# Optimization experiments

Hardware: AMD Instinct MI355X
Metric: run time of the kernel (lower is better)

Reference implementation:

```python
import jax, jax.numpy as jnp
import numpy as np

D_MODEL = 1024
K_QUERY = 32
K_TOPK = 4

def setup_inputs() -> dict:
    key = jax.random.key(0)
    k1, k2, k3, k4, k5 = jax.random.split(key, 5)
    x = jax.random.normal(k1, (4, 2048, D_MODEL), dtype=jnp.float32)
    # nn.Linear(d_model, k_query): weight [k_query, d_model], bias [k_query]
    sc = 1.0 / np.sqrt(D_MODEL)
    Wq = jax.random.uniform(k2, (K_QUERY, D_MODEL), jnp.float32, -sc, sc)
    bq = jax.random.uniform(k3, (K_QUERY,), jnp.float32, -sc, sc)
    Wk = jax.random.uniform(k4, (K_QUERY, D_MODEL), jnp.float32, -sc, sc)
    bk = jax.random.uniform(k5, (K_QUERY,), jnp.float32, -sc, sc)
    return {"x": x, "Wq": Wq, "bq": bq, "Wk": Wk, "bk": bk}

def reference(x, Wq, bq, Wk, bk):
    # x: [B, T, D]
    queries = jnp.einsum('btd,kd->btk', x, Wq) + bq      # [B, T, Kq]
    keys = jnp.einsum('btd,kd->btk', x, Wk) + bk         # [B, T, Kq]
    sim = jnp.einsum('btk,bsk->bts', queries, keys)      # [B, T, T]
    sim = sim / jnp.sqrt(jnp.float32(queries.shape[-1]))
    _, topk_idx = jax.lax.top_k(sim, K_TOPK)              # [B, T, K]
    # gather neighbors per (b, t): x[b, topk_idx[b, t]] -> [B, T, K, D]
    neighbors = jax.vmap(lambda xb, ib: xb[ib])(x, topk_idx)
    gathered = neighbors.mean(axis=2)                     # [B, T, D]
    return gathered
```

## Files before the change

kernel.cpp:

```cpp
#include <hip/hip_runtime.h>
#include <math.h>

#define D_MODEL 1024
#define T_SEQ   2048
#define NBATCH  4
#define NROWS   (NBATCH * T_SEQ)
#define NOUT    64
#define NQTR    4

#define SKLD 264
#define SQLD 36
#define XLD  1032

typedef double v4df __attribute__((ext_vector_type(4)));

__device__ __forceinline__ bool key_gt(float av, int ai, float bv, int bi) {
    return (av > bv) || (av == bv && ai < bi);
}

__device__ __forceinline__ void cmpswap(float& v0, int& i0, float& v1, int& i1) {
    bool sw = key_gt(v1, i1, v0, i0);
    float nv0 = sw ? v1 : v0, nv1 = sw ? v0 : v1;
    int   ni0 = sw ? i1 : i0, ni1 = sw ? i0 : i1;
    v0 = nv0; v1 = nv1; i0 = ni0; i1 = ni1;
}

__device__ __forceinline__ void merge4(float (&a)[4], int (&ai)[4],
                                       float b0, int j0, float b1, int j1,
                                       float b2, int j2, float b3, int j3) {
    if (!key_gt(a[0], ai[0], b3, j3)) { a[0] = b3; ai[0] = j3; }
    if (!key_gt(a[1], ai[1], b2, j2)) { a[1] = b2; ai[1] = j2; }
    if (!key_gt(a[2], ai[2], b1, j1)) { a[2] = b1; ai[2] = j1; }
    if (!key_gt(a[3], ai[3], b0, j0)) { a[3] = b0; ai[3] = j0; }
    cmpswap(a[0], ai[0], a[2], ai[2]);
    cmpswap(a[1], ai[1], a[3], ai[3]);
    cmpswap(a[0], ai[0], a[1], ai[1]);
    cmpswap(a[2], ai[2], a[3], ai[3]);
}

__device__ __forceinline__ void insert4(float (&tv)[4], int (&tix)[4], float v, int idx) {
    if (v > tv[3]) {
        bool g0 = v > tv[0], g1 = v > tv[1], g2 = v > tv[2];
        float n0 = g0 ? v : tv[0];
        int   m0 = g0 ? idx : tix[0];
        float n1 = g1 ? (g0 ? tv[0] : v) : tv[1];
        int   m1 = g1 ? (g0 ? tix[0] : idx) : tix[1];
        float n2 = g2 ? (g1 ? tv[1] : v) : tv[2];
        int   m2 = g2 ? (g1 ? tix[1] : idx) : tix[2];
        float n3 = g2 ? tv[2] : v;
        int   m3 = g2 ? tix[2] : idx;
        tv[0] = n0; tv[1] = n1; tv[2] = n2; tv[3] = n3;
        tix[0] = m0; tix[1] = m1; tix[2] = m2; tix[3] = m3;
    }
}

__global__ __launch_bounds__(64) void mfma_probe(int* __restrict__ tab)
{
    __shared__ double Aref[16][4];
    __shared__ double Bref[4][16];
    __shared__ double Dref[16][16];

    const int lane = threadIdx.x;
    {
        const int m = lane & 15, k = lane >> 4;
        Aref[m][k] = (double)(1 + m * 4 + k);
        Bref[k][m] = (double)(1 + k * 16 + m);
    }
    __syncthreads();
    for (int e = lane; e < 256; e += 64) {
        const int m = e >> 4, n = e & 15;
        double s = 0.0;
        for (int k = 0; k < 4; ++k) s += Aref[m][k] * Bref[k][n];
        Dref[m][n] = s;
    }
    __syncthreads();

    int found = -1;
    for (int h = 0; h < 16; ++h) {
        if (found >= 0) break;
        const int fa = h & 1, fb = (h >> 1) & 1, fd = h >> 2;
        const int am = fa ? (lane >> 2) : (lane & 15);
        const int ak = fa ? (lane & 3)  : (lane >> 4);
        const int bn = fb ? (lane >> 2) : (lane & 15);
        const int bk = fb ? (lane & 3)  : (lane >> 4);
        v4df c = {0.0, 0.0, 0.0, 0.0};
        c = __builtin_amdgcn_mfma_f64_16x16x4f64(Aref[am][ak], Bref[bk][bn], c, 0, 0, 0);
        bool ok = true;
        #pragma unroll
        for (int i = 0; i < 4; ++i) {
            int dm, dn;
            if (fd == 0)      { dm = 4 * (lane >> 4) + i; dn = lane & 15; }
            else if (fd == 1) { dn = 4 * (lane >> 4) + i; dm = lane & 15; }
            else if (fd == 2) { dm = (lane >> 4) + 4 * i; dn = lane & 15; }
            else              { dn = (lane >> 4) + 4 * i; dm = lane & 15; }
            if (c[i] != Dref[dm][dn]) ok = false;
        }
        if (__all(ok)) found = h;
    }

    const int fa = (found >= 0) ? (found & 1) : 0;
    const int fb = (found >= 0) ? ((found >> 1) & 1) : 0;
    const int fd = (found >= 0) ? (found >> 2) : 0;
    tab[1   + lane] = fa ? (lane >> 2) : (lane & 15);
    tab[65  + lane] = fa ? (lane & 3)  : (lane >> 4);
    tab[129 + lane] = fb ? (lane & 3)  : (lane >> 4);
    tab[193 + lane] = fb ? (lane >> 2) : (lane & 15);
    #pragma unroll
    for (int i = 0; i < 4; ++i) {
        int dm, dn;
        if (fd == 0)      { dm = 4 * (lane >> 4) + i; dn = lane & 15; }
        else if (fd == 1) { dn = 4 * (lane >> 4) + i; dm = lane & 15; }
        else if (fd == 2) { dm = (lane >> 4) + 4 * i; dn = lane & 15; }
        else              { dn = (lane >> 4) + 4 * i; dm = lane & 15; }
        tab[257 + lane * 4 + i] = dm;
        tab[513 + lane * 4 + i] = dn;
    }
    if (lane == 0) tab[0] = found;
}

__global__ __launch_bounds__(256) void wprep_kernel(
    const float* __restrict__ Wq, const float* __restrict__ Wk,
    double* __restrict__ Wdt)
{
    const int idx = blockIdx.x * 256 + threadIdx.x;
    const int o = idx & 63;
    const int d = idx >> 6;
    float v = (o < 32) ? Wq[(size_t)o * D_MODEL + d]
                       : Wk[(size_t)(o - 32) * D_MODEL + d];
    Wdt[(size_t)d * 64 + o] = (double)v;
}

__global__ __launch_bounds__(512) void proj_mfma(
    const float* __restrict__ x, const double* __restrict__ Wdt,
    const float* __restrict__ bq, const float* __restrict__ bk_,
    const int* __restrict__ tab,
    float* __restrict__ Qt, float* __restrict__ Kt)
{
    __shared__ float  xlds[16 * XLD];
    __shared__ double comb[4][64][4];

    const int tid  = threadIdx.x;
    const int lane = tid & 63;
    const int wav  = tid >> 6;
    const int og   = __builtin_amdgcn_readfirstlane(wav >> 1);
    const int half = __builtin_amdgcn_readfirstlane(wav & 1);
    const int row0 = blockIdx.x * 16;
    const int dbase = half * 512;

    const int flag = tab[0];
    const int am  = tab[1   + lane];
    const int ak  = tab[65  + lane];
    const int bkk = tab[129 + lane];
    const int bn  = tab[193 + lane];

    const double* wcol = Wdt + og * 16;

    #pragma unroll
    for (int j = 0; j < 8; ++j) {
        const int f  = j * 512 + tid;
        const int r  = f >> 8;
        const int c4 = f & 255;
        float4 v = *reinterpret_cast<const float4*>(
            x + (size_t)(row0 + r) * D_MODEL + c4 * 4);
        *reinterpret_cast<float4*>(&xlds[r * XLD + c4 * 4]) = v;
    }
    __syncthreads();

    v4df acc = {0.0, 0.0, 0.0, 0.0};

    if (flag >= 0) {
        #pragma unroll 8
        for (int kk = 0; kk < 128; ++kk) {
            double a = (double)xlds[am * XLD + dbase + kk * 4 + ak];
            double b = wcol[(size_t)(dbase + kk * 4 + bkk) * 64 + bn];
            acc = __builtin_amdgcn_mfma_f64_16x16x4f64(a, b, acc, 0, 0, 0);
        }
    } else {
        const int n  = lane & 15;
        const int r4 = (lane >> 4) * 4;
        for (int dd = 0; dd < 512; ++dd) {
            const int d = dbase + dd;
            double wv = wcol[(size_t)d * 64 + n];
            #pragma unroll
            for (int i = 0; i < 4; ++i)
                acc[i] = fma((double)xlds[(r4 + i) * XLD + d], wv, acc[i]);
        }
    }

    if (half == 1) {
        #pragma unroll
        for (int i = 0; i < 4; ++i) comb[og][lane][i] = acc[i];
    }
    __syncthreads();

    if (half == 0) {
        #pragma unroll
        for (int i = 0; i < 4; ++i) {
            const double tot = acc[i] + comb[og][lane][i];
            const int dmv = tab[257 + lane * 4 + i];
            const int dnv = tab[513 + lane * 4 + i];
            const int out = og * 16 + dnv;
            const int row = row0 + dmv;
            const int bb  = row >> 11, t = row & 2047;
            const double bias = (out < 32) ? (double)bq[out] : (double)bk_[out - 32];
            const float v = (float)(tot + bias);
            if (out < 32) Qt[((size_t)bb * 32 + out) * T_SEQ + t] = v;
            else          Kt[((size_t)bb * 32 + (out - 32)) * T_SEQ + t] = v;
        }
    }
}

__global__ __launch_bounds__(256) void sim_topk(
    const float* __restrict__ Qt, const float* __restrict__ Kt,
    float* __restrict__ candVal ,
    int*   __restrict__ candIdx )
{
    __shared__ float klds[32 * SKLD];
    __shared__ float qlds[32 * SQLD];
    __shared__ float cV[4][32][4];
    __shared__ int   cI[4][32][4];

    const int tid  = threadIdx.x;
    const int lane = tid & 63;
    const int wav  = tid >> 6;
    const int qtr  = blockIdx.x & 3;
    const int tt   = (blockIdx.x >> 2) & 63;
    const int b    = blockIdx.x >> 8;
    const int tblk = tt * 32;
    const int sq0  = qtr * 512;

    const float* QtB = Qt + (size_t)b * 32 * T_SEQ;
    const float* KtB = Kt + (size_t)b * 32 * T_SEQ;

    {
        const int i  = tid >> 3;
        const int t4 = (tid & 7) * 4;
        float4 v = *reinterpret_cast<const float4*>(QtB + (size_t)i * T_SEQ + tblk + t4);
        *reinterpret_cast<float4*>(&qlds[i * SQLD + t4]) = v;
    }

    const int t0 = (tid & 7) * 4;
    const int s0 = (tid >> 3) * 8;

    float tv[4][4]; int tix[4][4];
    #pragma unroll
    for (int r = 0; r < 4; ++r)
        #pragma unroll
        for (int j = 0; j < 4; ++j) { tv[r][j] = -INFINITY; tix[r][j] = 0x7fffffff; }

    for (int st = 0; st < 2; ++st) {
        __syncthreads();
        #pragma unroll
        for (int j = 0; j < 8; ++j) {
            const int f  = (tid + j * 256) * 4;
            const int ki = f >> 8;
            const int ks = f & 255;
            float4 v = *reinterpret_cast<const float4*>(
                KtB + (size_t)ki * T_SEQ + sq0 + st * 256 + ks);
            *reinterpret_cast<float4*>(&klds[ki * SKLD + ks]) = v;
        }
        __syncthreads();

        float acc[4][8];
        #pragma unroll
        for (int r = 0; r < 4; ++r)
            #pragma unroll
            for (int c = 0; c < 8; ++c) acc[r][c] = 0.f;

        #pragma unroll 4
        for (int i = 0; i < 32; ++i) {
            float4 qv  = *reinterpret_cast<const float4*>(&qlds[i * SQLD + t0]);
            float4 kv0 = *reinterpret_cast<const float4*>(&klds[i * SKLD + s0]);
            float4 kv1 = *reinterpret_cast<const float4*>(&klds[i * SKLD + s0 + 4]);
            const float qa[4] = {qv.x, qv.y, qv.z, qv.w};
            const float ka[8] = {kv0.x, kv0.y, kv0.z, kv0.w, kv1.x, kv1.y, kv1.z, kv1.w};
            #pragma unroll
            for (int r = 0; r < 4; ++r)
                #pragma unroll
                for (int c = 0; c < 8; ++c)
                    acc[r][c] = fmaf(qa[r], ka[c], acc[r][c]);
        }

        const int sbase = sq0 + st * 256 + s0;
        #pragma unroll
        for (int c = 0; c < 8; ++c)
            #pragma unroll
            for (int r = 0; r < 4; ++r)
                insert4(tv[r], tix[r], acc[r][c], sbase + c);
    }

    #pragma unroll
    for (int m = 8; m <= 32; m <<= 1) {
        #pragma unroll
        for (int r = 0; r < 4; ++r) {
            float b0 = __shfl_xor(tv[r][0], m, 64);
            float b1 = __shfl_xor(tv[r][1], m, 64);
            float b2 = __shfl_xor(tv[r][2], m, 64);
            float b3 = __shfl_xor(tv[r][3], m, 64);
            int   j0 = __shfl_xor(tix[r][0], m, 64);
            int   j1 = __shfl_xor(tix[r][1], m, 64);
            int   j2 = __shfl_xor(tix[r][2], m, 64);
            int   j3 = __shfl_xor(tix[r][3], m, 64);
            merge4(tv[r], tix[r], b0, j0, b1, j1, b2, j2, b3, j3);
        }
    }

    if (lane < 8) {
        #pragma unroll
        for (int r = 0; r < 4; ++r)
            #pragma unroll
            for (int j = 0; j < 4; ++j) {
                cV[wav][lane * 4 + r][j] = tv[r][j];
                cI[wav][lane * 4 + r][j] = tix[r][j];
            }
    }
    __syncthreads();

    if (tid < 32) {
        float mv[4]; int mi[4];
        #pragma unroll
        for (int j = 0; j < 4; ++j) { mv[j] = cV[0][tid][j]; mi[j] = cI[0][tid][j]; }
        #pragma unroll
        for (int w = 1; w < 4; ++w)
            merge4(mv, mi,
                   cV[w][tid][0], cI[w][tid][0],
                   cV[w][tid][1], cI[w][tid][1],
                   cV[w][tid][2], cI[w][tid][2],
                   cV[w][tid][3], cI[w][tid][3]);
        const size_t row = (size_t)b * T_SEQ + tblk + tid;
        float4 vv = {mv[0], mv[1], mv[2], mv[3]};
        int4   ii = {mi[0], mi[1], mi[2], mi[3]};
        *reinterpret_cast<float4*>(candVal + ((size_t)qtr * NROWS + row) * 4) = vv;
        *reinterpret_cast<int4*>(candIdx + ((size_t)qtr * NROWS + row) * 4) = ii;
    }
}

__global__ __launch_bounds__(256) void merge_gather(
    const float* __restrict__ x,
    const float* __restrict__ candVal, const int* __restrict__ candIdx,
    float* __restrict__ out)
{
    __shared__ int topIdx[8][4];

    const int tid  = threadIdx.x;
    const int row0 = blockIdx.x * 8;
    const int b    = row0 >> 11;

    if (tid < 8) {
        const size_t row = row0 + tid;
        float4 v0 = *reinterpret_cast<const float4*>(candVal + row * 4);
        int4   i0 = *reinterpret_cast<const int4*>(candIdx + row * 4);
        float mv[4] = {v0.x, v0.y, v0.z, v0.w};
        int   mi[4] = {i0.x, i0.y, i0.z, i0.w};
        #pragma unroll
        for (int q = 1; q < NQTR; ++q) {
            float4 v1 = *reinterpret_cast<const float4*>(candVal + ((size_t)q * NROWS + row) * 4);
            int4   i1 = *reinterpret_cast<const int4*>(candIdx + ((size_t)q * NROWS + row) * 4);
            merge4(mv, mi, v1.x, i1.x, v1.y, i1.y, v1.z, i1.z, v1.w, i1.w);
        }
        #pragma unroll
        for (int j = 0; j < 4; ++j) topIdx[tid][j] = mi[j];
    }
    __syncthreads();

    const float* xb = x + (size_t)b * T_SEQ * D_MODEL;
    float* ob = out + (size_t)row0 * D_MODEL;
    #pragma unroll
    for (int r = 0; r < 8; ++r) {
        const int i0 = topIdx[r][0], i1 = topIdx[r][1], i2 = topIdx[r][2], i3 = topIdx[r][3];
        float4 a0 = *(reinterpret_cast<const float4*>(xb + (size_t)i0 * D_MODEL) + tid);
        float4 a1 = *(reinterpret_cast<const float4*>(xb + (size_t)i1 * D_MODEL) + tid);
        float4 a2 = *(reinterpret_cast<const float4*>(xb + (size_t)i2 * D_MODEL) + tid);
        float4 a3 = *(reinterpret_cast<const float4*>(xb + (size_t)i3 * D_MODEL) + tid);
        float4 o;
        o.x = (a0.x + a1.x + a2.x + a3.x) * 0.25f;
        o.y = (a0.y + a1.y + a2.y + a3.y) * 0.25f;
        o.z = (a0.z + a1.z + a2.z + a3.z) * 0.25f;
        o.w = (a0.w + a1.w + a2.w + a3.w) * 0.25f;
        *(reinterpret_cast<float4*>(ob + (size_t)r * D_MODEL) + tid) = o;
    }
}

extern "C" void kernel_launch(void* const* d_in, const int* in_sizes, int n_in,
                              void* d_out, int out_size, void* d_ws, size_t ws_size,
                              hipStream_t stream) {
    const float* x  = (const float*)d_in[0];
    const float* Wq = (const float*)d_in[1];
    const float* bq = (const float*)d_in[2];
    const float* Wk = (const float*)d_in[3];
    const float* bk = (const float*)d_in[4];
    float* out = (float*)d_out;

    char* wsb = (char*)d_ws;
    int*    tab  = (int*)wsb;
    double* Wdt  = (double*)(wsb + 4096);
    float*  Qt   = (float*)(wsb + 4096 + (size_t)D_MODEL * NOUT * 8);
    float*  Kt   = Qt + (size_t)NBATCH * 32 * T_SEQ;
    float*  candVal = (float*)((char*)Kt + (size_t)NBATCH * 32 * T_SEQ * 4);
    int*    candIdx = (int*)((char*)candVal + (size_t)NQTR * NROWS * 4 * 4);

    mfma_probe<<<dim3(1), dim3(64), 0, stream>>>(tab);
    wprep_kernel<<<dim3(256), dim3(256), 0, stream>>>(Wq, Wk, Wdt);
    proj_mfma<<<dim3(NROWS / 16), dim3(512), 0, stream>>>(x, Wdt, bq, bk, tab, Qt, Kt);
    sim_topk<<<dim3(1024), dim3(256), 0, stream>>>(Qt, Kt, candVal, candIdx);
    merge_gather<<<dim3(1024), dim3(256), 0, stream>>>(x, candVal, candIdx, out);
}
```

Measured before the change: 163.9 us.

## Fuse probe into weight prep and merge+gather into sim_topk via last-block counter

```diff
diff --git a/kernel.cpp b/kernel.cpp
--- a/kernel.cpp
+++ b/kernel.cpp
@@ -54,26 +54,29 @@
     }
 }
 
-__global__ __launch_bounds__(64) void mfma_probe(int* __restrict__ tab)
+__device__ void run_probe(int tid, int* __restrict__ tab)
 {
     __shared__ double Aref[16][4];
     __shared__ double Bref[4][16];
     __shared__ double Dref[16][16];
 
-    const int lane = threadIdx.x;
-    {
+    const int lane = tid;
+    if (tid < 64) {
         const int m = lane & 15, k = lane >> 4;
         Aref[m][k] = (double)(1 + m * 4 + k);
         Bref[k][m] = (double)(1 + k * 16 + m);
     }
     __syncthreads();
-    for (int e = lane; e < 256; e += 64) {
+    {
+        const int e = tid;
         const int m = e >> 4, n = e & 15;
         double s = 0.0;
         for (int k = 0; k < 4; ++k) s += Aref[m][k] * Bref[k][n];
         Dref[m][n] = s;
     }
     __syncthreads();
+
+    if (tid >= 64) return;
 
     int found = -1;
     for (int h = 0; h < 16; ++h) {
@@ -118,16 +121,20 @@
     if (lane == 0) tab[0] = found;
 }
 
-__global__ __launch_bounds__(256) void wprep_kernel(
+__global__ __launch_bounds__(256) void wprep_probe(
     const float* __restrict__ Wq, const float* __restrict__ Wk,
-    double* __restrict__ Wdt)
+    double* __restrict__ Wdt, int* __restrict__ tab, int* __restrict__ cnt)
 {
-    const int idx = blockIdx.x * 256 + threadIdx.x;
+    const int tid = threadIdx.x;
+    const int idx = blockIdx.x * 256 + tid;
     const int o = idx & 63;
     const int d = idx >> 6;
     float v = (o < 32) ? Wq[(size_t)o * D_MODEL + d]
                        : Wk[(size_t)(o - 32) * D_MODEL + d];
     Wdt[(size_t)d * 64 + o] = (double)v;
+
+    if (blockIdx.x == 1) cnt[tid] = 0;
+    if (blockIdx.x == 0) run_probe(tid, tab);
 }
 
 __global__ __launch_bounds__(512) void proj_mfma(
@@ -210,15 +217,20 @@
     }
 }
 
-__global__ __launch_bounds__(256) void sim_topk(
+__global__ __launch_bounds__(256, 4) void sim_topk_gather(
+    const float* __restrict__ x,
     const float* __restrict__ Qt, const float* __restrict__ Kt,
     float* __restrict__ candVal ,
-    int*   __restrict__ candIdx )
+    int*   __restrict__ candIdx ,
+    int*   __restrict__ cnt     ,
+    float* __restrict__ out)
 {
     __shared__ float klds[32 * SKLD];
     __shared__ float qlds[32 * SQLD];
-    __shared__ float cV[4][32][4];
-    __shared__ int   cI[4][32][4];
+    float (*cV)[32][4] = reinterpret_cast<float(*)[32][4]>(klds);
+    int   (*cI)[32][4] = reinterpret_cast<int(*)[32][4]>(klds + 512);
+    int   (*topIdx)[4] = reinterpret_cast<int(*)[4]>(klds + 1024);
+    int*   lastFlag    = reinterpret_cast<int*>(klds + 1152);
 
     const int tid  = threadIdx.x;
     const int lane = tid & 63;
@@ -305,6 +317,8 @@
         }
     }
 
+    __syncthreads();
+
     if (lane < 8) {
         #pragma unroll
         for (int r = 0; r < 4; ++r)
@@ -333,21 +347,19 @@
         *reinterpret_cast<float4*>(candVal + ((size_t)qtr * NROWS + row) * 4) = vv;
         *reinterpret_cast<int4*>(candIdx + ((size_t)qtr * NROWS + row) * 4) = ii;
     }
-}
-
-__global__ __launch_bounds__(256) void merge_gather(
-    const float* __restrict__ x,
-    const float* __restrict__ candVal, const int* __restrict__ candIdx,
-    float* __restrict__ out)
-{
-    __shared__ int topIdx[8][4];
-
-    const int tid  = threadIdx.x;
-    const int row0 = blockIdx.x * 8;
-    const int b    = row0 >> 11;
-
-    if (tid < 8) {
-        const size_t row = row0 + tid;
+
+    __threadfence();
+    __syncthreads();
+    if (tid == 0) {
+        int old = atomicAdd(cnt + ((b << 6) | tt), 1);
+        *lastFlag = (old == 3);
+    }
+    __syncthreads();
+    if (!*lastFlag) return;
+    __threadfence();
+
+    if (tid < 32) {
+        const size_t row = (size_t)b * T_SEQ + tblk + tid;
         float4 v0 = *reinterpret_cast<const float4*>(candVal + row * 4);
         int4   i0 = *reinterpret_cast<const int4*>(candIdx + row * 4);
         float mv[4] = {v0.x, v0.y, v0.z, v0.w};
@@ -364,9 +376,9 @@
     __syncthreads();
 
     const float* xb = x + (size_t)b * T_SEQ * D_MODEL;
-    float* ob = out + (size_t)row0 * D_MODEL;
-    #pragma unroll
-    for (int r = 0; r < 8; ++r) {
+    float* ob = out + ((size_t)b * T_SEQ + tblk) * D_MODEL;
+    #pragma unroll 4
+    for (int r = 0; r < 32; ++r) {
         const int i0 = topIdx[r][0], i1 = topIdx[r][1], i2 = topIdx[r][2], i3 = topIdx[r][3];
         float4 a0 = *(reinterpret_cast<const float4*>(xb + (size_t)i0 * D_MODEL) + tid);
         float4 a1 = *(reinterpret_cast<const float4*>(xb + (size_t)i1 * D_MODEL) + tid);
@@ -398,10 +410,9 @@
     float*  Kt   = Qt + (size_t)NBATCH * 32 * T_SEQ;
     float*  candVal = (float*)((char*)Kt + (size_t)NBATCH * 32 * T_SEQ * 4);
     int*    candIdx = (int*)((char*)candVal + (size_t)NQTR * NROWS * 4 * 4);
-
-    mfma_probe<<<dim3(1), dim3(64), 0, stream>>>(tab);
-    wprep_kernel<<<dim3(256), dim3(256), 0, stream>>>(Wq, Wk, Wdt);
+    int*    cnt     = (int*)((char*)candIdx + (size_t)NQTR * NROWS * 4 * 4);
+
+    wprep_probe<<<dim3(256), dim3(256), 0, stream>>>(Wq, Wk, Wdt, tab, cnt);
     proj_mfma<<<dim3(NROWS / 16), dim3(512), 0, stream>>>(x, Wdt, bq, bk, tab, Qt, Kt);
-    sim_topk<<<dim3(1024), dim3(256), 0, stream>>>(Qt, Kt, candVal, candIdx);
-    merge_gather<<<dim3(1024), dim3(256), 0, stream>>>(x, candVal, candIdx, out);
-}
+    sim_topk_gather<<<dim3(1024), dim3(256), 0, stream>>>(x, Qt, Kt, candVal, candIdx, cnt, out);
+}
```

Result: slower. 293.1 us (+78.9%).
